# Optimization experiments

Measured on AMD Instinct MI355X. Metric: run time of the kernel, lower is better.

Reference implementation:

```python
import jax, jax.numpy as jnp
import numpy as np
from jax import lax

DN2 = ('NCHW', 'OIHW', 'NCHW')
DN3 = ('NCDHW', 'OIDHW', 'NCDHW')


def _convlstm_step(h, c, x, W, b):
    # x: [B, Cin, H, W], h/c: [B, nf, H, W], W: [4*nf, Cin+nf, 3, 3]
    comb = jnp.concatenate([x, h], axis=1)
    cc = lax.conv_general_dilated(comb, W, (1, 1), 'SAME', dimension_numbers=DN2)
    cc = cc + b[None, :, None, None]
    ci, cf, co, cg = jnp.split(cc, 4, axis=1)
    i = jax.nn.sigmoid(ci)
    f = jax.nn.sigmoid(cf)
    o = jax.nn.sigmoid(co)
    g = jnp.tanh(cg)
    c_next = f * c + i * g
    h_next = o * jnp.tanh(c_next)
    return h_next, c_next


def setup_inputs() -> dict:
    key = jax.random.key(0)
    ks = jax.random.split(key, 4)
    B, T, Cin, H, W = 32, 12, 1, 64, 64
    nf = 64
    s = 0.05
    return {
        'x': jax.random.normal(ks[0], (B, T, Cin, H, W), jnp.float32),
        'future_step': 12,
        'W_enc': jax.random.normal(ks[1], (4 * nf, Cin + nf, 3, 3), jnp.float32) * s,
        'b_enc': jnp.zeros((4 * nf,), jnp.float32),
        'W_dec': jax.random.normal(ks[2], (4 * nf, nf + nf, 3, 3), jnp.float32) * s,
        'b_dec': jnp.zeros((4 * nf,), jnp.float32),
        'W_cnn': jax.random.normal(ks[3], (1, nf, 1, 3, 3), jnp.float32) * s,
        'b_cnn': jnp.zeros((1,), jnp.float32),
    }


def reference(x, future_step, W_enc, b_enc, W_dec, b_dec, W_cnn, b_cnn):
    B, T, Cin, H, Wd = x.shape
    nf = W_enc.shape[0] // 4
    h0 = jnp.zeros((B, nf, H, Wd), x.dtype)
    c0 = jnp.zeros((B, nf, H, Wd), x.dtype)

    # ---- encoder: scan over time ----
    def enc_step(carry, xt):
        h, c = carry
        h, c = _convlstm_step(h, c, xt, W_enc, b_enc)
        return (h, c), None

    (h_t, _), _ = lax.scan(enc_step, (h0, c0), jnp.moveaxis(x, 1, 0))
    encoder_vector = h_t
    out_encoder_vector = encoder_vector.reshape(B, -1)

    # ---- decoder: feed back h as next input ----
    def dec_step(carry, _):
        ev, h, c = carry
        h, c = _convlstm_step(h, c, ev, W_dec, b_dec)
        return (h, h, c), h

    _, outs = lax.scan(dec_step, (encoder_vector, h0, c0), None, length=future_step)
    # outs: [Tf, B, nf, H, W] -> [B, nf, Tf, H, W]
    outs = jnp.transpose(outs, (1, 2, 0, 3, 4))

    # ---- 3D CNN head: kernel (1,3,3), padding (0,1,1) ----
    y = lax.conv_general_dilated(outs, W_cnn, (1, 1, 1),
                                 [(0, 0), (1, 1), (1, 1)],
                                 dimension_numbers=DN3)
    y = y + b_cnn[None, :, None, None, None]
    # [B, 1, Tf, H, W] -> [B, Tf, 1, H, W]
    y = jnp.transpose(y, (0, 2, 1, 3, 4))
    return y, out_encoder_vector
```

## Files before the change

### kernel.cpp

```cpp
#include <hip/hip_runtime.h>
#include <hip/hip_bf16.h>


#define HW 4096
#define NF 64

typedef __attribute__((ext_vector_type(8))) short bf16x8;
typedef __attribute__((ext_vector_type(4))) float f32x4;

__device__ __forceinline__ float fsig(float v) {
  return __builtin_amdgcn_rcpf(1.f + __expf(-v));
}
__device__ __forceinline__ float ftanh(float v) {
  float vc = fminf(fmaxf(v, -15.f), 15.f);
  float e = __expf(2.f * vc);
  return (e - 1.f) * __builtin_amdgcn_rcpf(e + 1.f);
}
__device__ __forceinline__ float bf2f(short s) {
  union { unsigned u; float f; } a;
  a.u = ((unsigned)(unsigned short)s) << 16;
  return a.f;
}
__device__ __forceinline__ short f2bf(float f) {
  union { float f; unsigned u; } a;
  a.f = f;
  unsigned r = (a.u + 0x7fff + ((a.u >> 16) & 1)) >> 16;
  return (short)r;
}
__device__ __forceinline__ void dma16(const short* g, short* l) {
  __builtin_amdgcn_global_load_lds(
      (const __attribute__((address_space(1))) char*)g,
      (__attribute__((address_space(3))) char*)l, 16, 0, 0);
}

template <bool HAS_X>
__global__ __launch_bounds__(512) void lstm_mfma_k(
    const short* __restrict__ hin,
    const short* __restrict__ W,
    const float* __restrict__ wx,
    const float* __restrict__ xpl,
    const float* __restrict__ bias,
    const float* __restrict__ cin,
    const short* __restrict__ zbuf,
    short* __restrict__ hout,
    float* __restrict__ cout) {
  const int b = blockIdx.x;
  const int y = blockIdx.y;
  const int tid = threadIdx.x;
  const int lane = tid & 63;
  const int wv = tid >> 6;
  const int wnf = wv & 3;
  const int whalf = wv >> 2;
  const int col = lane & 15;
  const int quad = lane >> 4;

  __shared__ short As2[2][8192];
  __shared__ short Bs[3 * 66 * 64];
  __shared__ float xs[3][64];

  const short* hb = hin + (size_t)b * (HW * 64);
#pragma unroll
  for (int r = 0; r < 3; ++r) {
    const int py = y - 1 + r;
    const short* src = (py >= 0 && py < 64)
        ? hb + ((py * 64 + 8 * wv + (lane >> 3)) * 64 + (lane & 7) * 8)
        : zbuf + lane * 8;
    dma16(src, &Bs[(r * 66 + 8 * wv + 1) * 64]);
  }
  dma16(W + (wv * 64 + lane) * 8, &As2[0][wv * 64 * 8]);
  dma16(W + (512 + wv * 64 + lane) * 8, &As2[0][(512 + wv * 64) * 8]);
  if (tid < 48) {
    const int r = tid >> 4;
    const int s = ((tid >> 3) & 1) * 65;
    const int ch0 = (tid & 7) * 8;
    bf16x8 z = {0, 0, 0, 0, 0, 0, 0, 0};
    *reinterpret_cast<bf16x8*>(&Bs[(r * 66 + s) * 64 + ch0]) = z;
  }
  if (HAS_X) {
    if (tid < 192) {
      const float* xb = xpl + (size_t)b * (12 * HW);
      const int r = tid >> 6, cx = tid & 63;
      const int py = y - 1 + r;
      xs[r][cx] = (py >= 0 && py < 64) ? xb[py * 64 + cx] : 0.f;
    }
  }
  __syncthreads();

  dma16(W + 8192 + (wv * 64 + lane) * 8, &As2[1][wv * 64 * 8]);
  dma16(W + 8192 + (512 + wv * 64 + lane) * 8, &As2[1][(512 + wv * 64) * 8]);

  f32x4 acc[4][2];
#pragma unroll
  for (int g = 0; g < 4; ++g) {
    const int oc0 = g * 64 + wnf * 16 + quad * 4;
#pragma unroll
    for (int nt = 0; nt < 2; ++nt)
#pragma unroll
      for (int r = 0; r < 4; ++r) acc[g][nt][r] = bias[oc0 + r];
  }

  if (HAS_X) {
#pragma unroll
    for (int nt = 0; nt < 2; ++nt) {
      const int px = whalf * 32 + nt * 16 + col;
#pragma unroll
      for (int tap = 0; tap < 9; ++tap) {
        const int pxx = px + (tap % 3) - 1;
        const float xv = (pxx >= 0 && pxx < 64) ? xs[tap / 3][pxx] : 0.f;
#pragma unroll
        for (int g = 0; g < 4; ++g) {
          const int oc0 = g * 64 + wnf * 16 + quad * 4;
#pragma unroll
          for (int r = 0; r < 4; ++r)
            acc[g][nt][r] = fmaf(xv, wx[(oc0 + r) * 9 + tap], acc[g][nt][r]);
        }
      }
    }
  }

  const int axr = (col & 7) << 3;
#pragma unroll
  for (int k = 0; k < 18; ++k) {
    const int tap = k >> 1, gp = k & 1, p = k & 1;
    if (k > 0) {
      __syncthreads();
      if (k < 17) {
        const int nk = k + 1;
        const short* src = W + (nk >> 1) * 16384 + (nk & 1) * 8192;
        dma16(src + (wv * 64 + lane) * 8, &As2[nk & 1][wv * 64 * 8]);
        dma16(src + (512 + wv * 64 + lane) * 8, &As2[nk & 1][(512 + wv * 64) * 8]);
      }
    }
    const int hr = tap / 3;
    const int sb = col + tap % 3;
    const int sx = (sb & 7) << 3;
    const int srow = (hr * 66 + whalf * 32 + sb) * 64;
#pragma unroll
    for (int kc = 0; kc < 2; ++kc) {
      const int chb = kc * 32 + quad * 8;
      const int abase = ((wnf * 16 + col) * 64 + chb) ^ axr;
      const int bbase = (srow + chb) ^ sx;
      bf16x8 a0 = *reinterpret_cast<const bf16x8*>(&As2[p][abase]);
      bf16x8 a1 = *reinterpret_cast<const bf16x8*>(&As2[p][abase + 4096]);
      bf16x8 b0 = *reinterpret_cast<const bf16x8*>(&Bs[bbase]);
      bf16x8 b1 = *reinterpret_cast<const bf16x8*>(&Bs[bbase + 1024]);
      __builtin_amdgcn_s_setprio(1);
      acc[gp * 2][0] = __builtin_amdgcn_mfma_f32_16x16x32_bf16(a0, b0, acc[gp * 2][0], 0, 0, 0);
      acc[gp * 2][1] = __builtin_amdgcn_mfma_f32_16x16x32_bf16(a0, b1, acc[gp * 2][1], 0, 0, 0);
      acc[gp * 2 + 1][0] = __builtin_amdgcn_mfma_f32_16x16x32_bf16(a1, b0, acc[gp * 2 + 1][0], 0, 0, 0);
      acc[gp * 2 + 1][1] = __builtin_amdgcn_mfma_f32_16x16x32_bf16(a1, b1, acc[gp * 2 + 1][1], 0, 0, 0);
      __builtin_amdgcn_s_setprio(0);
    }
  }

  const int nf0 = wnf * 16 + quad * 4;
#pragma unroll
  for (int nt = 0; nt < 2; ++nt) {
    const int px = whalf * 32 + nt * 16 + col;
    const int swz = ((px + 1) & 7) << 3;
    const size_t pix = (size_t)b * HW + y * 64 + px;
    f32x4 cold = *reinterpret_cast<const f32x4*>(cin + pix * 64 + nf0);
    f32x4 cnew;
    short hnew[4];
#pragma unroll
    for (int r = 0; r < 4; ++r) {
      float i_ = fsig(acc[0][nt][r]);
      float f_ = fsig(acc[1][nt][r]);
      float o_ = fsig(acc[2][nt][r]);
      float g_ = ftanh(acc[3][nt][r]);
      float cn = fmaf(f_, cold[r], i_ * g_);
      cnew[r] = cn;
      hnew[r] = f2bf(o_ * ftanh(cn));
    }
    *reinterpret_cast<f32x4*>(cout + pix * 64 + nf0) = cnew;
    short4 hv = make_short4(hnew[0], hnew[1], hnew[2], hnew[3]);
    *reinterpret_cast<short4*>(hout + pix * 64 + (nf0 ^ swz)) = hv;
  }
}

__global__ __launch_bounds__(256) void head_k(const short* __restrict__ h,
                                              const float* __restrict__ wc2,
                                              const float* __restrict__ bc,
                                              float* __restrict__ yout, int t) {
  const int tid = blockIdx.x * 256 + threadIdx.x;
  const int pix = tid & 4095;
  const int b = tid >> 12;
  const int x0 = pix & 63, y0 = pix >> 6;
  float acc = bc[0];
  const short* hb = h + (size_t)b * (HW * 64);
#pragma unroll
  for (int tap = 0; tap < 9; ++tap) {
    const int yy = y0 + tap / 3 - 1, xx = x0 + (tap % 3) - 1;
    if (yy < 0 || yy > 63 || xx < 0 || xx > 63) continue;
    const short* hp = hb + (yy * 64 + xx) * 64;
    const int sw8 = (xx + 1) & 7;
    const float* wp = wc2 + tap * 64;
#pragma unroll
    for (int f8 = 0; f8 < 8; ++f8) {
      bf16x8 v = *reinterpret_cast<const bf16x8*>(hp + ((f8 ^ sw8) * 8));
#pragma unroll
      for (int j = 0; j < 8; ++j) acc = fmaf(wp[f8 * 8 + j], bf2f(v[j]), acc);
    }
  }
  yout[(size_t)(b * 12 + t) * HW + pix] = acc;
}

__global__ __launch_bounds__(256) void ev_out_k(const short* __restrict__ h,
                                                float* __restrict__ out) {
  __shared__ float tl[64][65];
  const int b = blockIdx.y, pg = blockIdx.x;
  const int p0 = pg * 64;
  {
    const int pixl = threadIdx.x >> 2, c0 = (threadIdx.x & 3) * 16;
    const int sw8 = (pixl + 1) & 7;
    const short* hp = h + ((size_t)b * HW + p0 + pixl) * 64;
#pragma unroll
    for (int gi = 0; gi < 2; ++gi) {
      const int grp = (c0 >> 3) + gi;
      bf16x8 v = *reinterpret_cast<const bf16x8*>(hp + ((grp ^ sw8) * 8));
#pragma unroll
      for (int j = 0; j < 8; ++j) tl[pixl][grp * 8 + j] = bf2f(v[j]);
    }
  }
  __syncthreads();
  {
    const int ch = threadIdx.x >> 2, q0 = (threadIdx.x & 3) * 16;
    float* op = out + ((size_t)b * 64 + ch) * (size_t)HW + p0 + q0;
#pragma unroll
    for (int i = 0; i < 16; ++i) op[i] = tl[q0 + i][ch];
  }
}

__global__ __launch_bounds__(256) void reo_enc_k(const float* __restrict__ src,
                                                 short* __restrict__ Wh,
                                                 float* __restrict__ wx) {
  const int idx = blockIdx.x * 256 + threadIdx.x;
  if (idx < 9 * 256 * 64) {
    const int tap = idx >> 14, oc = (idx >> 6) & 255, c = idx & 63;
    const int dst = tap * 16384 + (((oc * 64) + c) ^ ((oc & 7) << 3));
    Wh[dst] = f2bf(src[(oc * 65 + (c + 1)) * 9 + tap]);
  }
  if (idx < 256 * 9) {
    const int oc = idx / 9, tap = idx % 9;
    wx[idx] = src[(oc * 65 + 0) * 9 + tap];
  }
}

__global__ __launch_bounds__(256) void reo_dec_k(const float* __restrict__ src,
                                                 short* __restrict__ Wx,
                                                 short* __restrict__ Ws) {
  const int idx = blockIdx.x * 256 + threadIdx.x;
  if (idx >= 9 * 256 * 64) return;
  const int tap = idx >> 14, oc = (idx >> 6) & 255, c = idx & 63;
  const int dst = tap * 16384 + (((oc * 64) + c) ^ ((oc & 7) << 3));
  const float a = src[(oc * 128 + c) * 9 + tap];
  const float b = src[(oc * 128 + 64 + c) * 9 + tap];
  Wx[dst] = f2bf(a);
  Ws[dst] = f2bf(a + b);
}

__global__ __launch_bounds__(256) void reo_cnn_k(const float* __restrict__ src,
                                                 float* __restrict__ wc2) {
  const int idx = blockIdx.x * 256 + threadIdx.x;
  if (idx >= 576) return;
  wc2[idx] = src[(idx % 64) * 9 + (idx / 64)];
}

extern "C" void kernel_launch(void* const* d_in, const int* in_sizes, int n_in,
                              void* d_out, int out_size, void* d_ws, size_t ws_size,
                              hipStream_t stream) {
  const float* x = (const float*)d_in[0];
  const float* W_enc = (const float*)d_in[2];
  const float* b_enc = (const float*)d_in[3];
  const float* W_dec = (const float*)d_in[4];
  const float* b_dec = (const float*)d_in[5];
  const float* W_cnn = (const float*)d_in[6];
  const float* b_cnn = (const float*)d_in[7];
  float* out = (float*)d_out;
  float* out_y = out;
  float* out_ev = out + 1572864;

  float* ws = (float*)d_ws;
  float* cA = ws;
  float* cB = cA + 8388608;
  short* hA = (short*)(cB + 8388608);
  short* hB = hA + 8388608;
  short* WEh = hB + 8388608;
  short* WDx = WEh + 147456;
  short* WDs = WDx + 147456;
  float* wx = (float*)(WDs + 147456);
  float* wc2 = wx + 2304;
  short* zb = (short*)(wc2 + 576);

  reo_enc_k<<<(147456 + 255) / 256, 256, 0, stream>>>(W_enc, WEh, wx);
  reo_dec_k<<<(147456 + 255) / 256, 256, 0, stream>>>(W_dec, WDx, WDs);
  reo_cnn_k<<<3, 256, 0, stream>>>(W_cnn, wc2);

  hipMemsetAsync(hA, 0, 8388608 * sizeof(short), stream);
  hipMemsetAsync(cA, 0, 8388608 * sizeof(float), stream);
  hipMemsetAsync(zb, 0, 512 * sizeof(short), stream);

  dim3 gridL(32, 64), blkL(512);
  dim3 gridE(64, 32), blkE(256);
  short *ha = hA, *hb = hB;
  float *ca = cA, *cb = cB;

  for (int t = 0; t < 12; ++t) {
    lstm_mfma_k<true><<<gridL, blkL, 0, stream>>>(ha, WEh, wx, x + t * HW,
                                                  b_enc, ca, zb, hb, cb);
    { short* tm = ha; ha = hb; hb = tm; }
    { float* tm = ca; ca = cb; cb = tm; }
  }
  ev_out_k<<<gridE, blkE, 0, stream>>>(ha, out_ev);

  hipMemsetAsync(cb, 0, 8388608 * sizeof(float), stream);
  { float* tm = ca; ca = cb; cb = tm; }

  for (int t = 0; t < 12; ++t) {
    lstm_mfma_k<false><<<gridL, blkL, 0, stream>>>(
        ha, (t == 0) ? WDx : WDs, nullptr, nullptr, b_dec, ca, zb, hb, cb);
    { short* tm = ha; ha = hb; hb = tm; }
    { float* tm = ca; ca = cb; cb = tm; }
    head_k<<<512, 256, 0, stream>>>(ha, wc2, b_cnn, out_y, t);
  }
}
```

Measured before the change: 1.943 ms.

## Triple-buffer weight tiles with prefetch distance two and vmcnt-based waits

Replaces the double-buffered LDS weight tile with a three-slot ring, issuing DMA loads two k-steps ahead. The full __syncthreads is replaced by explicit s_waitcnt vmcnt counts plus s_barrier, so only the oldest outstanding load must land before each step. The aim is to hide global-to-LDS latency of the weight stream behind MFMA work. It costs 16KB more LDS per block, which may reduce occupancy, and relies on hand-counted vmcnt values being correct.

```diff
diff --git a/kernel.cpp b/kernel.cpp
--- a/kernel.cpp
+++ b/kernel.cpp
@@ -54,7 +54,7 @@
   const int col = lane & 15;
   const int quad = lane >> 4;
 
-  __shared__ short As2[2][8192];
+  __shared__ short As3[3][8192];
   __shared__ short Bs[3 * 66 * 64];
   __shared__ float xs[3][64];
 
@@ -67,8 +67,12 @@
         : zbuf + lane * 8;
     dma16(src, &Bs[(r * 66 + 8 * wv + 1) * 64]);
   }
-  dma16(W + (wv * 64 + lane) * 8, &As2[0][wv * 64 * 8]);
-  dma16(W + (512 + wv * 64 + lane) * 8, &As2[0][(512 + wv * 64) * 8]);
+#pragma unroll
+  for (int k = 0; k < 2; ++k) {
+    const short* src = W + (k >> 1) * 16384 + (k & 1) * 8192;
+    dma16(src + (wv * 64 + lane) * 8, &As3[k][wv * 64 * 8]);
+    dma16(src + (512 + wv * 64 + lane) * 8, &As3[k][(512 + wv * 64) * 8]);
+  }
   if (tid < 48) {
     const int r = tid >> 4;
     const int s = ((tid >> 3) & 1) * 65;
@@ -84,10 +88,8 @@
       xs[r][cx] = (py >= 0 && py < 64) ? xb[py * 64 + cx] : 0.f;
     }
   }
-  __syncthreads();
-
-  dma16(W + 8192 + (wv * 64 + lane) * 8, &As2[1][wv * 64 * 8]);
-  dma16(W + 8192 + (512 + wv * 64 + lane) * 8, &As2[1][(512 + wv * 64) * 8]);
+  asm volatile("s_waitcnt vmcnt(2) lgkmcnt(0)" ::: "memory");
+  __builtin_amdgcn_s_barrier();
 
   f32x4 acc[4][2];
 #pragma unroll
@@ -121,15 +123,19 @@
   const int axr = (col & 7) << 3;
 #pragma unroll
   for (int k = 0; k < 18; ++k) {
-    const int tap = k >> 1, gp = k & 1, p = k & 1;
+    const int tap = k >> 1, gp = k & 1, p = k % 3;
     if (k > 0) {
-      __syncthreads();
-      if (k < 17) {
-        const int nk = k + 1;
-        const short* src = W + (nk >> 1) * 16384 + (nk & 1) * 8192;
-        dma16(src + (wv * 64 + lane) * 8, &As2[nk & 1][wv * 64 * 8]);
-        dma16(src + (512 + wv * 64 + lane) * 8, &As2[nk & 1][(512 + wv * 64) * 8]);
-      }
+      if (k == 17)
+        asm volatile("s_waitcnt vmcnt(0)" ::: "memory");
+      else
+        asm volatile("s_waitcnt vmcnt(2)" ::: "memory");
+      __builtin_amdgcn_s_barrier();
+    }
+    if (k + 2 < 18) {
+      const int nk = k + 2;
+      const short* src = W + (nk >> 1) * 16384 + (nk & 1) * 8192;
+      dma16(src + (wv * 64 + lane) * 8, &As3[nk % 3][wv * 64 * 8]);
+      dma16(src + (512 + wv * 64 + lane) * 8, &As3[nk % 3][(512 + wv * 64) * 8]);
     }
     const int hr = tap / 3;
     const int sb = col + tap % 3;
@@ -140,8 +146,8 @@
       const int chb = kc * 32 + quad * 8;
       const int abase = ((wnf * 16 + col) * 64 + chb) ^ axr;
       const int bbase = (srow + chb) ^ sx;
-      bf16x8 a0 = *reinterpret_cast<const bf16x8*>(&As2[p][abase]);
-      bf16x8 a1 = *reinterpret_cast<const bf16x8*>(&As2[p][abase + 4096]);
+      bf16x8 a0 = *reinterpret_cast<const bf16x8*>(&As3[p][abase]);
+      bf16x8 a1 = *reinterpret_cast<const bf16x8*>(&As3[p][abase + 4096]);
       bf16x8 b0 = *reinterpret_cast<const bf16x8*>(&Bs[bbase]);
       bf16x8 b1 = *reinterpret_cast<const bf16x8*>(&Bs[bbase + 1024]);
       __builtin_amdgcn_s_setprio(1);
```

Result: no change. 1.940 ms (-0.2%).
